# Kernel tuning notes

Hardware: AMD Instinct MI355X
Metric: run time of the kernel (lower is better)

## Reference

```python
import jax, jax.numpy as jnp
import numpy as np
import math

EPS = 1e-7
K_NEIGHBORS = 32  # matches init kwarg k

def _project(x, c):
    norm = jnp.linalg.norm(x, axis=-1, keepdims=True).clip(EPS)
    sqrt_c = jnp.sqrt(c).clip(EPS)
    max_norm = (1.0 - EPS) / sqrt_c
    return x * jnp.minimum(max_norm / norm, 1.0)

def _mobius_add(x, y, c):
    x2 = jnp.sum(x * x, axis=-1, keepdims=True)
    y2 = jnp.sum(y * y, axis=-1, keepdims=True)
    xy = jnp.sum(x * y, axis=-1, keepdims=True)
    num = (1 + 2 * c * xy + c * y2) * x + (1 - c * x2) * y
    den = 1 + 2 * c * xy + c * c * x2 * y2
    return _project(num / den.clip(EPS), c)

def _dist(x, y, c):
    sqrt_c = jnp.sqrt(c).clip(EPS)
    diff = _mobius_add(x, -y, c)
    dn = jnp.linalg.norm(diff, axis=-1)
    arg = jnp.minimum(sqrt_c * dn.clip(EPS, 1 - EPS), 1.0 - EPS)
    return 2.0 * jnp.arctanh(arg) / sqrt_c

def _logmap0(y, c):
    sqrt_c = jnp.sqrt(c).clip(EPS)
    yn = jnp.linalg.norm(y, axis=-1, keepdims=True)
    is_zero = yn < EPS
    syn = yn.clip(EPS)
    arg = jnp.minimum(sqrt_c * syn, 1.0 - EPS)
    mag = jnp.arctanh(arg) / sqrt_c
    return jnp.where(is_zero, jnp.zeros_like(y), mag * y / syn)

def _layernorm(x, g, b):
    m = x.mean(-1, keepdims=True)
    v = x.var(-1, keepdims=True)
    return (x - m) / jnp.sqrt(v + 1e-6) * g + b

def setup_inputs() -> dict:
    key = jax.random.key(0)
    B, N, D, P, H = 2, 2048, 512, 3, 8
    ks = jax.random.split(key, 16)
    s = 0.02
    d = {}
    d['x'] = jax.random.normal(ks[0], (B, N, D), dtype=jnp.float32)
    d['positions'] = jax.random.normal(ks[1], (B, N, P), dtype=jnp.float32) * 0.1
    d['c'] = jnp.float32(1.0)
    d['Wq'] = jax.random.normal(ks[2], (D, D), jnp.float32) * s; d['bq'] = jnp.zeros((D,), jnp.float32)
    d['Wk'] = jax.random.normal(ks[3], (D, D), jnp.float32) * s; d['bk'] = jnp.zeros((D,), jnp.float32)
    d['Wv'] = jax.random.normal(ks[4], (D, D), jnp.float32) * s; d['bv'] = jnp.zeros((D,), jnp.float32)
    d['Wg'] = jax.random.normal(ks[5], (P, D), jnp.float32) * s; d['bg'] = jnp.zeros((D,), jnp.float32)
    d['Wo'] = jax.random.normal(ks[6], (D, D), jnp.float32) * s; d['bo'] = jnp.zeros((D,), jnp.float32)
    d['Wf1'] = jax.random.normal(ks[7], (D, 4 * D), jnp.float32) * s; d['bf1'] = jnp.zeros((4 * D,), jnp.float32)
    d['Wf2'] = jax.random.normal(ks[8], (4 * D, D), jnp.float32) * s; d['bf2'] = jnp.zeros((D,), jnp.float32)
    d['g1'] = jnp.ones((D,), jnp.float32); d['b1'] = jnp.zeros((D,), jnp.float32)
    d['g2'] = jnp.ones((D,), jnp.float32); d['b2'] = jnp.zeros((D,), jnp.float32)
    d['ascale'] = jnp.ones((H,), jnp.float32)
    d['fscale'] = jnp.ones((H,), jnp.float32)
    return d

def reference(x, positions, c, Wq, bq, Wk, bk, Wv, bv, Wg, bg, Wo, bo, Wf1, bf1, Wf2, bf2, g1, b1, g2, b2, ascale, fscale):
    B, N, D = x.shape
    H = ascale.shape[0]
    hd = D // H
    K = K_NEIGHBORS

    xn = _layernorm(x, g1, b1)
    q = (xn @ Wq + bq).reshape(B, N, H, hd)
    k = (xn @ Wk + bk).reshape(B, N, H, hd)
    v = (xn @ Wv + bv).reshape(B, N, H, hd)

    # full pairwise hyperbolic distance matrix [B, N, N]
    dmat = _dist(positions[:, :, None, :], positions[:, None, :, :], c)
    idx = jax.lax.top_k(-dmat, K)[1]  # [B, N, K]

    bidx = jnp.arange(B)[:, None, None]
    key_pos = positions[bidx, idx]                 # [B, N, K, P]
    qpos = positions[:, :, None, :]                # [B, N, 1, P]
    geo = _logmap0(_mobius_add(-qpos, key_pos, c), c)
    geo_v = (geo @ Wg + bg).reshape(B, N, K, H, hd)

    kg = k[bidx, idx]                              # [B, N, K, H, hd]
    vg = v[bidx, idx]

    align = jnp.einsum('bnhd,bnkhd->bhnk', q, geo_v)
    feat = jnp.einsum('bnhd,bnkhd->bhnk', q, kg) / math.sqrt(hd)
    scores = fscale[None, :, None, None] * feat + ascale[None, :, None, None] * align
    w = jax.nn.softmax(scores.astype(jnp.float32), axis=-1)
    attn = jnp.einsum('bhnk,bnkhd->bnhd', w, vg).reshape(B, N, D)

    x1 = x + attn @ Wo + bo
    h = _layernorm(x1, g2, b2)
    x2 = x1 + jax.nn.gelu(h @ Wf1 + bf1) @ Wf2 + bf2
    return x2
```

## Files before the change

### kernel.cpp

```cpp
#include <hip/hip_runtime.h>
#include <math.h>

#define EPSF 1e-7f

constexpr int Bb = 2, Nn = 2048, Dd = 512, Hh = 8, HD = 64, KK = 32;
constexpr int ROWS = Bb * Nn;

typedef __attribute__((ext_vector_type(8))) short bf16x8;
typedef __attribute__((ext_vector_type(4))) float f32x4;
typedef __attribute__((ext_vector_type(8))) unsigned short u16x8;
typedef unsigned long long u64;

__device__ inline unsigned short f2bf(float f) {
    union { float f; unsigned int u; } v; v.f = f;
    unsigned int u = v.u;
    unsigned int r = (u + 0x7fffu + ((u >> 16) & 1u)) >> 16;
    return (unsigned short)r;
}

__device__ inline float bf2f(short s) {
    union { unsigned int u; float f; } x;
    x.u = ((unsigned int)(unsigned short)s) << 16;
    return x.f;
}

__device__ inline float gelu_tanh(float v) {
    float u = v + 0.044715f * v * v * v;
    return 0.5f * v * (1.f + tanhf(0.79788456080286535588f * u));
}

__device__ __forceinline__ void tcvt(float (*tile)[65], const float* __restrict__ in,
                                     unsigned short* __restrict__ out,
                                     int K, int N, int bx, int by) {
    int k0 = by * 64, n0 = bx * 64;
    int t = threadIdx.x;
    int lr = t >> 6, lc = t & 63;
#pragma unroll 4
    for (int p = 0; p < 16; ++p) {
        int r = p * 4 + lr;
        tile[r][lc] = in[(size_t)(k0 + r) * N + n0 + lc];
    }
    __syncthreads();
#pragma unroll 4
    for (int p = 0; p < 16; ++p) {
        int n = p * 4 + lr;
        out[(size_t)(n0 + n) * K + k0 + lc] = f2bf(tile[lc][n]);
    }
}

__device__ __forceinline__ void ln_row(const float* __restrict__ x,
                                       const float* __restrict__ g,
                                       const float* __restrict__ b,
                                       unsigned short* __restrict__ out,
                                       int row, int lane) {
    const float* xr = x + (size_t)row * Dd;
    float4 v0 = *(const float4*)(xr + lane * 8);
    float4 v1 = *(const float4*)(xr + lane * 8 + 4);
    float s = v0.x + v0.y + v0.z + v0.w + v1.x + v1.y + v1.z + v1.w;
    float s2 = v0.x * v0.x + v0.y * v0.y + v0.z * v0.z + v0.w * v0.w +
               v1.x * v1.x + v1.y * v1.y + v1.z * v1.z + v1.w * v1.w;
    for (int o = 32; o; o >>= 1) { s += __shfl_xor(s, o); s2 += __shfl_xor(s2, o); }
    float mean = s * (1.f / Dd);
    float var = s2 * (1.f / Dd) - mean * mean;
    float rstd = rsqrtf(var + 1e-6f);
    float4 g0 = *(const float4*)(g + lane * 8);
    float4 g1v = *(const float4*)(g + lane * 8 + 4);
    float4 b0 = *(const float4*)(b + lane * 8);
    float4 b1v = *(const float4*)(b + lane * 8 + 4);
    u16x8 o;
    o[0] = f2bf((v0.x - mean) * rstd * g0.x + b0.x);
    o[1] = f2bf((v0.y - mean) * rstd * g0.y + b0.y);
    o[2] = f2bf((v0.z - mean) * rstd * g0.z + b0.z);
    o[3] = f2bf((v0.w - mean) * rstd * g0.w + b0.w);
    o[4] = f2bf((v1.x - mean) * rstd * g1v.x + b1v.x);
    o[5] = f2bf((v1.y - mean) * rstd * g1v.y + b1v.y);
    o[6] = f2bf((v1.z - mean) * rstd * g1v.z + b1v.z);
    o[7] = f2bf((v1.w - mean) * rstd * g1v.w + b1v.w);
    *(u16x8*)(out + (size_t)row * Dd + lane * 8) = o;
}

__global__ __launch_bounds__(256) void ln_kernel(const float* __restrict__ x,
                                                 const float* __restrict__ g,
                                                 const float* __restrict__ b,
                                                 unsigned short* __restrict__ out) {
    ln_row(x, g, b, out, blockIdx.x * 4 + (threadIdx.x >> 6), threadIdx.x & 63);
}

__global__ __launch_bounds__(256) void prep_kernel(
    const float* __restrict__ Wq, const float* __restrict__ Wk,
    const float* __restrict__ Wv, const float* __restrict__ Wo,
    const float* __restrict__ Wf1, const float* __restrict__ Wf2,
    const float* __restrict__ bq, const float* __restrict__ bk, const float* __restrict__ bv,
    const float* __restrict__ x, const float* __restrict__ g1, const float* __restrict__ b1,
    unsigned short* __restrict__ wqkv_t, unsigned short* __restrict__ wo_t,
    unsigned short* __restrict__ wf1_t, unsigned short* __restrict__ wf2_t,
    float* __restrict__ bqkv, unsigned short* __restrict__ xn) {
    __shared__ float tile[64][65];
    int bid = blockIdx.x;
    if (bid < 256) {
        int z = bid >> 6, r = bid & 63;
        const float* in = (z == 0) ? Wq : (z == 1) ? Wk : (z == 2) ? Wv : Wo;
        unsigned short* out = (z == 0) ? wqkv_t : (z == 1) ? wqkv_t + 262144
                            : (z == 2) ? wqkv_t + 524288 : wo_t;
        tcvt(tile, in, out, 512, 512, r & 7, r >> 3);
    } else if (bid < 512) {
        int r = bid - 256;
        tcvt(tile, Wf1, wf1_t, 512, 2048, r & 31, r >> 5);
    } else if (bid < 768) {
        int r = bid - 512;
        tcvt(tile, Wf2, wf2_t, 2048, 512, r & 7, r >> 3);
    } else if (bid < 774) {
        int t = (bid - 768) * 256 + threadIdx.x;
        if (t < 512) bqkv[t] = bq[t];
        else if (t < 1024) bqkv[t] = bk[t - 512];
        else if (t < 1536) bqkv[t] = bv[t - 1024];
    } else {
        ln_row(x, g1, b1, xn, (bid - 774) * 4 + (threadIdx.x >> 6), threadIdx.x & 63);
    }
}

template <int EPI, int OBF16>
__global__ __launch_bounds__(256) void gemm64(const unsigned short* __restrict__ A,
                                              const unsigned short* __restrict__ Bt,
                                              const float* __restrict__ bias,
                                              const float* __restrict__ resid,
                                              void* __restrict__ C,
                                              int N, int K, int gridX) {
    __shared__ short As[2 * 64 * 64];
    __shared__ short Bs[2 * 64 * 64];
    int nwg = gridDim.x;
    int cpx = nwg >> 3;
    int wgid = blockIdx.x;
    int nid = (wgid & 7) * cpx + (wgid >> 3);
    int bx = nid % gridX, by = nid / gridX;
    int bm = by * 64, bn = bx * 64;
    int tid = threadIdx.x;
    int wave = tid >> 6, lane = tid & 63;
    int wr = wave >> 1, wc = wave & 1;
    f32x4 acc[2][2] = {};

    int srow = wave * 8 + (lane >> 3);
    int scol = ((lane & 7) ^ (lane >> 3)) * 8;
    const unsigned short* gA0 = A + (size_t)(bm + srow) * K + scol;
    const unsigned short* gA1 = A + (size_t)(bm + srow + 32) * K + scol;
    const unsigned short* gB0 = Bt + (size_t)(bn + srow) * K + scol;
    const unsigned short* gB1 = Bt + (size_t)(bn + srow + 32) * K + scol;

#define STAGE(buf, kof)                                                                                 \
    do {                                                                                                \
        __builtin_amdgcn_global_load_lds((const __attribute__((address_space(1))) void*)(gA0 + (kof)), \
            (__attribute__((address_space(3))) void*)(As + (buf) * 4096 + wave * 512), 16, 0, 0);       \
        __builtin_amdgcn_global_load_lds((const __attribute__((address_space(1))) void*)(gA1 + (kof)), \
            (__attribute__((address_space(3))) void*)(As + (buf) * 4096 + 2048 + wave * 512), 16, 0, 0);\
        __builtin_amdgcn_global_load_lds((const __attribute__((address_space(1))) void*)(gB0 + (kof)), \
            (__attribute__((address_space(3))) void*)(Bs + (buf) * 4096 + wave * 512), 16, 0, 0);       \
        __builtin_amdgcn_global_load_lds((const __attribute__((address_space(1))) void*)(gB1 + (kof)), \
            (__attribute__((address_space(3))) void*)(Bs + (buf) * 4096 + 2048 + wave * 512), 16, 0, 0);\
    } while (0)

    int nt = K >> 6;
    int cur = 0;
    STAGE(0, 0);
    __syncthreads();
    for (int t = 0; t < nt; ++t) {
        if (t + 1 < nt) STAGE(cur ^ 1, (t + 1) * 64);
        const short* as = As + cur * 4096;
        const short* bs = Bs + cur * 4096;
#pragma unroll
        for (int kk = 0; kk < 64; kk += 32) {
            int kx = (kk + (lane >> 4) * 8) ^ ((lane & 7) << 3);
            bf16x8 a0 = *(const bf16x8*)(as + (wr * 32 + (lane & 15)) * 64 + kx);
            bf16x8 a1 = *(const bf16x8*)(as + (wr * 32 + 16 + (lane & 15)) * 64 + kx);
            bf16x8 b0 = *(const bf16x8*)(bs + (wc * 32 + (lane & 15)) * 64 + kx);
            bf16x8 b1 = *(const bf16x8*)(bs + (wc * 32 + 16 + (lane & 15)) * 64 + kx);
            acc[0][0] = __builtin_amdgcn_mfma_f32_16x16x32_bf16(a0, b0, acc[0][0], 0, 0, 0);
            acc[0][1] = __builtin_amdgcn_mfma_f32_16x16x32_bf16(a0, b1, acc[0][1], 0, 0, 0);
            acc[1][0] = __builtin_amdgcn_mfma_f32_16x16x32_bf16(a1, b0, acc[1][0], 0, 0, 0);
            acc[1][1] = __builtin_amdgcn_mfma_f32_16x16x32_bf16(a1, b1, acc[1][1], 0, 0, 0);
        }
        __syncthreads();
        cur ^= 1;
    }
#undef STAGE

    int cbase = bn + wc * 32 + (lane & 15);
    int rbase = bm + wr * 32 + (lane >> 4) * 4;
    float bias_v[2] = {bias[cbase], bias[cbase + 16]};
#pragma unroll
    for (int mi = 0; mi < 2; ++mi) {
#pragma unroll
        for (int r = 0; r < 4; ++r) {
            int row = rbase + mi * 16 + r;
#pragma unroll
            for (int ni = 0; ni < 2; ++ni) {
                int col = cbase + ni * 16;
                float v = acc[mi][ni][r] + bias_v[ni];
                if (EPI == 1) v += resid[(size_t)row * N + col];
                if (EPI == 2) v = gelu_tanh(v);
                if (OBF16) ((unsigned short*)C)[(size_t)row * N + col] = f2bf(v);
                else ((float*)C)[(size_t)row * N + col] = v;
            }
        }
    }
}

template <int CTRL>
__device__ inline float dpp_f(float v) {
    int i = __float_as_int(v);
    i = __builtin_amdgcn_update_dpp(i, i, CTRL, 0xF, 0xF, false);
    return __int_as_float(i);
}
template <int CTRL>
__device__ inline unsigned dpp_u(unsigned v) {
    return (unsigned)__builtin_amdgcn_update_dpp((int)v, (int)v, CTRL, 0xF, 0xF, false);
}

__device__ inline float wave_min_f32(float v) {
    v = fminf(v, dpp_f<0xB1>(v));
    v = fminf(v, dpp_f<0x4E>(v));
    v = fminf(v, dpp_f<0x141>(v));
    v = fminf(v, dpp_f<0x140>(v));
    v = fminf(v, __shfl_xor(v, 16));
    v = fminf(v, __shfl_xor(v, 32));
    return v;
}
__device__ inline unsigned wave_min_u32(unsigned v) {
    unsigned o;
    o = dpp_u<0xB1>(v);  v = o < v ? o : v;
    o = dpp_u<0x4E>(v);  v = o < v ? o : v;
    o = dpp_u<0x141>(v); v = o < v ? o : v;
    o = dpp_u<0x140>(v); v = o < v ? o : v;
    o = __shfl_xor(v, 16); v = o < v ? o : v;
    o = __shfl_xor(v, 32); v = o < v ? o : v;
    return v;
}

__global__ __launch_bounds__(256, 4) void topk_kernel(const float* __restrict__ pos,
                                                      const float* __restrict__ cp,
                                                      int* __restrict__ idx_out) {
    __shared__ float s_px[Nn], s_py[Nn], s_pz[Nn], s_u[Nn];
    __shared__ int s_out[4][KK];
    int b = blockIdx.x >> 9;
    int q0 = (blockIdx.x & 511) * 4;
    int t = threadIdx.x;
    float c = *cp;
    const float* pb = pos + (size_t)b * Nn * 3;
    for (int j = t; j < Nn; j += 256) {
        float px = pb[j * 3 + 0], py = pb[j * 3 + 1], pz = pb[j * 3 + 2];
        s_px[j] = px; s_py[j] = py; s_pz[j] = pz;
        s_u[j] = c * (px * px + py * py + pz * pz);
    }
    __syncthreads();
    int wave = t >> 6, lane = t & 63;
    int n = q0 + wave;
    float qx = s_px[n], qy = s_py[n], qz = s_pz[n];
    float cx2 = s_u[n];
    float x2 = cx2 / c;
    float B = 1.f - cx2;
    float rc = 1.f / c;
    float B2rc = B * B * rc;
    float m2c = -2.f * c;
    float m2B = -2.f * B;
    float key[32];
#pragma unroll
    for (int i = 0; i < 32; ++i) {
        int j = i * 64 + lane;
        float dot = qx * s_px[j] + qy * s_py[j] + qz * s_pz[j];
        float su = s_u[j];
        float r = fmaf(m2c, dot, 1.f);
        float A = r + su;
        float den = fmaf(cx2, su, r);
        float p1 = x2 * A;
        float q1 = A * dot;
        float t1 = fmaf(m2B, q1, B2rc * su);
        float num2 = fmaf(p1, A, t1);
        float rd = __builtin_amdgcn_rcpf(den);
        key[i] = fmaf(num2, rd * rd, 1.0f);
    }
    const u64 MAXK = ~0ull;
    u64 B0 = MAXK, B1 = MAXK, B2 = MAXK, B3 = MAXK;
#pragma unroll
    for (int i = 0; i < 32; ++i) {
        u64 k = ((u64)__float_as_uint(key[i]) << 32) | (unsigned int)(i * 64 + lane);
        if (k < B3) {
            B3 = k;
            if (B3 < B2) { u64 tmp = B2; B2 = B3; B3 = tmp; }
            if (B2 < B1) { u64 tmp = B1; B1 = B2; B2 = tmp; }
            if (B1 < B0) { u64 tmp = B0; B0 = B1; B1 = tmp; }
        }
    }
    int bcount = 4, consumed = 0;
    u64 last = 0;
    for (int s2 = 0; s2 < KK; ++s2) {
        bool need = (bcount == 0) && (consumed < 32);
        if (__any(need)) {
            if (need) {
                B0 = MAXK; B1 = MAXK; B2 = MAXK; B3 = MAXK;
#pragma unroll
                for (int i = 0; i < 32; ++i) {
                    u64 k = ((u64)__float_as_uint(key[i]) << 32) | (unsigned int)(i * 64 + lane);
                    if (k > last && k < B3) {
                        B3 = k;
                        if (B3 < B2) { u64 tmp = B2; B2 = B3; B3 = tmp; }
                        if (B2 < B1) { u64 tmp = B1; B1 = B2; B2 = tmp; }
                        if (B1 < B0) { u64 tmp = B0; B0 = B1; B1 = tmp; }
                    }
                }
                int rem = 32 - consumed;
                bcount = rem < 4 ? rem : 4;
            }
        }
        u64 offer = (bcount > 0) ? B0 : MAXK;
        float okey = __uint_as_float((unsigned)(offer >> 32));
        unsigned oidx = (unsigned)offer;
        float m = wave_min_f32(okey);
        u64 mask = __ballot(okey == m);
        unsigned gidx;
        if (__popcll(mask) == 1) {
            gidx = (unsigned)__shfl((int)oidx, __ffsll(mask) - 1);
        } else {
            unsigned cand = ((mask >> lane) & 1ull) ? oidx : 0xFFFFFFFFu;
            gidx = wave_min_u32(cand);
        }
        if (lane == 0) s_out[wave][s2] = (int)gidx;
        if (okey == m && oidx == gidx) {
            B0 = B1; B1 = B2; B2 = B3; B3 = MAXK;
            --bcount; ++consumed;
            last = ((u64)__float_as_uint(m) << 32) | gidx;
        }
    }
    if (lane < KK) idx_out[(size_t)(b * Nn + n) * KK + lane] = s_out[wave][lane];
}

__global__ __launch_bounds__(256) void attn_kernel(const unsigned short* __restrict__ qkv,
                                                   const int* __restrict__ idx,
                                                   const float* __restrict__ pos,
                                                   const float* __restrict__ Wg,
                                                   const float* __restrict__ bg,
                                                   const float* __restrict__ ascale,
                                                   const float* __restrict__ fscale,
                                                   const float* __restrict__ cp,
                                                   unsigned short* __restrict__ out) {
    constexpr int QS = 1536;
    int bid = blockIdx.x;
    int xcd = bid & 7, slot = bid >> 3;
    int b = xcd >> 2;
    int n = (xcd & 3) * 512 + slot;
    int bn = b * Nn + n;
    int t = threadIdx.x;
    int wave = t >> 6, lane = t & 63;
    __shared__ float s_q[Dd];
    __shared__ float s_geo[KK][3];
    __shared__ int s_idx[KK];
    __shared__ float s_qg[Hh][3];
    __shared__ float s_qb[Hh];
    __shared__ float s_dot[KK][9];
    __shared__ float s_w[Hh][KK];
    __shared__ float s_part[4][Dd];
    float c = *cp;
    if (t >= 64 && t < 96) s_idx[t - 64] = idx[(size_t)bn * KK + (t - 64)];
    if (t < 64) {
        bf16x8 q8 = *(const bf16x8*)(qkv + (size_t)bn * QS + t * 8);
#pragma unroll
        for (int j = 0; j < 8; ++j) s_q[t * 8 + j] = bf2f(q8[j]);
    }
    __syncthreads();
    if (t < KK) {
        const float* qp = pos + (size_t)bn * 3;
        const float* kp = pos + (size_t)(b * Nn + s_idx[t]) * 3;
        float xx = -qp[0], xyc = -qp[1], xz = -qp[2];
        float yx = kp[0], yy = kp[1], yz = kp[2];
        float x2 = xx * xx + xyc * xyc + xz * xz;
        float y2 = yx * yx + yy * yy + yz * yz;
        float xy = xx * yx + xyc * yy + xz * yz;
        float Av = 1.f + 2.f * c * xy + c * y2;
        float Bv = 1.f - c * x2;
        float den = fmaxf(1.f + 2.f * c * xy + c * c * x2 * y2, EPSF);
        float mx = (Av * xx + Bv * yx) / den;
        float my = (Av * xyc + Bv * yy) / den;
        float mz = (Av * xz + Bv * yz) / den;
        float rn = fmaxf(sqrtf(mx * mx + my * my + mz * mz), EPSF);
        float sqrt_c = fmaxf(sqrtf(c), EPSF);
        float max_norm = (1.f - EPSF) / sqrt_c;
        float scpr = fminf(max_norm / rn, 1.f);
        mx *= scpr; my *= scpr; mz *= scpr;
        float yn = sqrtf(mx * mx + my * my + mz * mz);
        if (yn < EPSF) {
            s_geo[t][0] = 0.f; s_geo[t][1] = 0.f; s_geo[t][2] = 0.f;
        } else {
            float syn = fmaxf(yn, EPSF);
            float arg = fminf(sqrt_c * syn, 1.f - EPSF);
            float mag = atanhf(arg) / sqrt_c;
            float f = mag / syn;
            s_geo[t][0] = mx * f; s_geo[t][1] = my * f; s_geo[t][2] = mz * f;
        }
    } else if (t >= 64 && t < 88) {
        int h = (t - 64) / 3, p = (t - 64) % 3;
        float acc = 0.f;
        for (int d2 = 0; d2 < HD; ++d2) acc += s_q[h * HD + d2] * Wg[p * Dd + h * HD + d2];
        s_qg[h][p] = acc;
    } else if (t >= 96 && t < 104) {
        int h = t - 96;
        float acc = 0.f;
        for (int d2 = 0; d2 < HD; ++d2) acc += s_q[h * HD + d2] * bg[h * HD + d2];
        s_qb[h] = acc;
    }
    bf16x8 v8r[8];
    {
#pragma unroll
        for (int r = 0; r < 8; ++r) {
            int kk = wave * 8 + r;
            int nk = s_idx[kk];
            bf16x8 k8 = *(const bf16x8*)(qkv + (size_t)(b * Nn + nk) * QS + 512 + lane * 8);
            float p = 0.f;
#pragma unroll
            for (int j = 0; j < 8; ++j) p = fmaf(bf2f(k8[j]), s_q[lane * 8 + j], p);
            p += __shfl_xor(p, 1);
            p += __shfl_xor(p, 2);
            p += __shfl_xor(p, 4);
            if ((lane & 7) == 0) s_dot[kk][lane >> 3] = p;
        }
#pragma unroll
        for (int r = 0; r < 8; ++r) {
            int nk = s_idx[wave * 8 + r];
            v8r[r] = *(const bf16x8*)(qkv + (size_t)(b * Nn + nk) * QS + 1024 + lane * 8);
        }
    }
    __syncthreads();
    {
        int h = t >> 5, kk = t & 31;
        float align = s_geo[kk][0] * s_qg[h][0] + s_geo[kk][1] * s_qg[h][1] +
                      s_geo[kk][2] * s_qg[h][2] + s_qb[h];
        float scv = fscale[h] * s_dot[kk][h] * 0.125f + ascale[h] * align;
        float m = scv;
        for (int o = 16; o; o >>= 1) m = fmaxf(m, __shfl_xor(m, o));
        float e = expf(scv - m);
        float ss = e;
        for (int o = 16; o; o >>= 1) ss += __shfl_xor(ss, o);
        s_w[h][kk] = e / ss;
    }
    __syncthreads();
    {
        float acc[8] = {0.f, 0.f, 0.f, 0.f, 0.f, 0.f, 0.f, 0.f};
        int h = lane >> 3;
#pragma unroll
        for (int r = 0; r < 8; ++r) {
            float wgt = s_w[h][wave * 8 + r];
#pragma unroll
            for (int j = 0; j < 8; ++j) acc[j] = fmaf(bf2f(v8r[r][j]), wgt, acc[j]);
        }
#pragma unroll
        for (int j = 0; j < 8; ++j) s_part[wave][lane * 8 + j] = acc[j];
    }
    __syncthreads();
    for (int d = t; d < Dd; d += 256) {
        float s = s_part[0][d] + s_part[1][d] + s_part[2][d] + s_part[3][d];
        out[(size_t)bn * Dd + d] = f2bf(s);
    }
}

extern "C" void kernel_launch(void* const* d_in, const int* in_sizes, int n_in,
                              void* d_out, int out_size, void* d_ws, size_t ws_size,
                              hipStream_t stream) {
    const float* x   = (const float*)d_in[0];
    const float* pos = (const float*)d_in[1];
    const float* cp  = (const float*)d_in[2];
    const float* Wq  = (const float*)d_in[3];
    const float* bq  = (const float*)d_in[4];
    const float* Wk  = (const float*)d_in[5];
    const float* bk  = (const float*)d_in[6];
    const float* Wv  = (const float*)d_in[7];
    const float* bv  = (const float*)d_in[8];
    const float* Wg  = (const float*)d_in[9];
    const float* bg  = (const float*)d_in[10];
    const float* Wo  = (const float*)d_in[11];
    const float* bo  = (const float*)d_in[12];
    const float* Wf1 = (const float*)d_in[13];
    const float* bf1 = (const float*)d_in[14];
    const float* Wf2 = (const float*)d_in[15];
    const float* bf2 = (const float*)d_in[16];
    const float* g1  = (const float*)d_in[17];
    const float* b1  = (const float*)d_in[18];
    const float* g2  = (const float*)d_in[19];
    const float* b2  = (const float*)d_in[20];
    const float* asc = (const float*)d_in[21];
    const float* fsc = (const float*)d_in[22];
    float* out = (float*)d_out;
    char* ws = (char*)d_ws;

    unsigned short* qkv_bf  = (unsigned short*)(ws + 0);
    unsigned short* t_bf    = (unsigned short*)(ws + 0);
    unsigned short* xn_bf   = (unsigned short*)(ws + 25165824);
    float*          x1      = (float*)(ws + 29360128);
    unsigned short* attn_bf = (unsigned short*)(ws + 37748736);
    unsigned short* wqkv_t  = (unsigned short*)(ws + 41943040);
    unsigned short* wo_t    = (unsigned short*)(ws + 43515904);
    unsigned short* wf1_t   = (unsigned short*)(ws + 44040192);
    unsigned short* wf2_t   = (unsigned short*)(ws + 46137344);
    int*            idx     = (int*)(ws + 48234496);
    float*          bqkv    = (float*)(ws + 48758784);

    prep_kernel<<<1798, 256, 0, stream>>>(Wq, Wk, Wv, Wo, Wf1, Wf2, bq, bk, bv,
                                          x, g1, b1, wqkv_t, wo_t, wf1_t, wf2_t, bqkv, xn_bf);
    topk_kernel<<<ROWS / 4, 256, 0, stream>>>(pos, cp, idx);
    gemm64<0, 1><<<1536, 256, 0, stream>>>(xn_bf, wqkv_t, bqkv, nullptr, qkv_bf, 1536, 512, 24);
    attn_kernel<<<ROWS, 256, 0, stream>>>(qkv_bf, idx, pos, Wg, bg, asc, fsc, cp, attn_bf);
    gemm64<1, 0><<<512, 256, 0, stream>>>(attn_bf, wo_t, bo, x, x1, 512, 512, 8);
    ln_kernel<<<ROWS / 4, 256, 0, stream>>>(x1, g2, b2, xn_bf);
    gemm64<2, 1><<<2048, 256, 0, stream>>>(xn_bf, wf1_t, bf1, nullptr, t_bf, 2048, 512, 32);
    gemm64<1, 0><<<512, 256, 0, stream>>>(t_bf, wf2_t, bf2, x1, out, 512, 2048, 8);
}
```

Baseline: 138.9 us.

## Fuse top-k into prep kernel and use 128x64 tiles for wide GEMMs

Merges the neighbor top-k selection into the weight-prep/layernorm launch as extra blocks, removing one kernel launch and letting the two independent stages run side by side. Adds a 128x64 GEMM tile variant, used for the QKV and FFN-up projections, so each A/B tile loaded into LDS feeds more MFMAs. The fused kernel now reserves about 33KB of shared memory for every block and sets a min-4-blocks launch bound, which may limit occupancy for the prep blocks. The larger tile halves the grid size and raises register pressure.

```diff
diff --git a/kernel.cpp b/kernel.cpp
--- a/kernel.cpp
+++ b/kernel.cpp
@@ -86,7 +86,138 @@
     ln_row(x, g, b, out, blockIdx.x * 4 + (threadIdx.x >> 6), threadIdx.x & 63);
 }
 
-__global__ __launch_bounds__(256) void prep_kernel(
+template <int CTRL>
+__device__ inline float dpp_f(float v) {
+    int i = __float_as_int(v);
+    i = __builtin_amdgcn_update_dpp(i, i, CTRL, 0xF, 0xF, false);
+    return __int_as_float(i);
+}
+template <int CTRL>
+__device__ inline unsigned dpp_u(unsigned v) {
+    return (unsigned)__builtin_amdgcn_update_dpp((int)v, (int)v, CTRL, 0xF, 0xF, false);
+}
+
+__device__ inline float wave_min_f32(float v) {
+    v = fminf(v, dpp_f<0xB1>(v));
+    v = fminf(v, dpp_f<0x4E>(v));
+    v = fminf(v, dpp_f<0x141>(v));
+    v = fminf(v, dpp_f<0x140>(v));
+    v = fminf(v, __shfl_xor(v, 16));
+    v = fminf(v, __shfl_xor(v, 32));
+    return v;
+}
+__device__ inline unsigned wave_min_u32(unsigned v) {
+    unsigned o;
+    o = dpp_u<0xB1>(v);  v = o < v ? o : v;
+    o = dpp_u<0x4E>(v);  v = o < v ? o : v;
+    o = dpp_u<0x141>(v); v = o < v ? o : v;
+    o = dpp_u<0x140>(v); v = o < v ? o : v;
+    o = __shfl_xor(v, 16); v = o < v ? o : v;
+    o = __shfl_xor(v, 32); v = o < v ? o : v;
+    return v;
+}
+
+__device__ __forceinline__ void topk_body(char* smem, const float* __restrict__ pos,
+                                          const float* __restrict__ cp,
+                                          int* __restrict__ idx_out, int bid) {
+    float* s_px = (float*)smem;
+    float* s_py = s_px + Nn;
+    float* s_pz = s_py + Nn;
+    float* s_u  = s_pz + Nn;
+    int* s_out  = (int*)(s_u + Nn);
+    int b = bid >> 9;
+    int q0 = (bid & 511) * 4;
+    int t = threadIdx.x;
+    float c = *cp;
+    const float* pb = pos + (size_t)b * Nn * 3;
+    for (int j = t; j < Nn; j += 256) {
+        float px = pb[j * 3 + 0], py = pb[j * 3 + 1], pz = pb[j * 3 + 2];
+        s_px[j] = px; s_py[j] = py; s_pz[j] = pz;
+        s_u[j] = c * (px * px + py * py + pz * pz);
+    }
+    __syncthreads();
+    int wave = t >> 6, lane = t & 63;
+    int n = q0 + wave;
+    float qx = s_px[n], qy = s_py[n], qz = s_pz[n];
+    float cx2 = s_u[n];
+    float x2 = cx2 / c;
+    float B = 1.f - cx2;
+    float rc = 1.f / c;
+    float B2rc = B * B * rc;
+    float m2c = -2.f * c;
+    float m2B = -2.f * B;
+    float key[32];
+#pragma unroll
+    for (int i = 0; i < 32; ++i) {
+        int j = i * 64 + lane;
+        float dot = qx * s_px[j] + qy * s_py[j] + qz * s_pz[j];
+        float su = s_u[j];
+        float r = fmaf(m2c, dot, 1.f);
+        float A = r + su;
+        float den = fmaf(cx2, su, r);
+        float p1 = x2 * A;
+        float q1 = A * dot;
+        float t1 = fmaf(m2B, q1, B2rc * su);
+        float num2 = fmaf(p1, A, t1);
+        float rd = __builtin_amdgcn_rcpf(den);
+        key[i] = fmaf(num2, rd * rd, 1.0f);
+    }
+    const u64 MAXK = ~0ull;
+    u64 B0 = MAXK, B1 = MAXK, B2 = MAXK, B3 = MAXK;
+#pragma unroll
+    for (int i = 0; i < 32; ++i) {
+        u64 k = ((u64)__float_as_uint(key[i]) << 32) | (unsigned int)(i * 64 + lane);
+        if (k < B3) {
+            B3 = k;
+            if (B3 < B2) { u64 tmp = B2; B2 = B3; B3 = tmp; }
+            if (B2 < B1) { u64 tmp = B1; B1 = B2; B2 = tmp; }
+            if (B1 < B0) { u64 tmp = B0; B0 = B1; B1 = tmp; }
+        }
+    }
+    int bcount = 4, consumed = 0;
+    u64 last = 0;
+    for (int s2 = 0; s2 < KK; ++s2) {
+        bool need = (bcount == 0) && (consumed < 32);
+        if (__any(need)) {
+            if (need) {
+                B0 = MAXK; B1 = MAXK; B2 = MAXK; B3 = MAXK;
+#pragma unroll
+                for (int i = 0; i < 32; ++i) {
+                    u64 k = ((u64)__float_as_uint(key[i]) << 32) | (unsigned int)(i * 64 + lane);
+                    if (k > last && k < B3) {
+                        B3 = k;
+                        if (B3 < B2) { u64 tmp = B2; B2 = B3; B3 = tmp; }
+                        if (B2 < B1) { u64 tmp = B1; B1 = B2; B2 = tmp; }
+                        if (B1 < B0) { u64 tmp = B0; B0 = B1; B1 = tmp; }
+                    }
+                }
+                int rem = 32 - consumed;
+                bcount = rem < 4 ? rem : 4;
+            }
+        }
+        u64 offer = (bcount > 0) ? B0 : MAXK;
+        float okey = __uint_as_float((unsigned)(offer >> 32));
+        unsigned oidx = (unsigned)offer;
+        float m = wave_min_f32(okey);
+        u64 mask = __ballot(okey == m);
+        unsigned gidx;
+        if (__popcll(mask) == 1) {
+            gidx = (unsigned)__shfl((int)oidx, __ffsll(mask) - 1);
+        } else {
+            unsigned cand = ((mask >> lane) & 1ull) ? oidx : 0xFFFFFFFFu;
+            gidx = wave_min_u32(cand);
+        }
+        if (lane == 0) s_out[wave * KK + s2] = (int)gidx;
+        if (okey == m && oidx == gidx) {
+            B0 = B1; B1 = B2; B2 = B3; B3 = MAXK;
+            --bcount; ++consumed;
+            last = ((u64)__float_as_uint(m) << 32) | gidx;
+        }
+    }
+    if (lane < KK) idx_out[(size_t)(b * Nn + n) * KK + lane] = s_out[wave * KK + lane];
+}
+
+__global__ __launch_bounds__(256, 4) void prep_topk_kernel(
     const float* __restrict__ Wq, const float* __restrict__ Wk,
     const float* __restrict__ Wv, const float* __restrict__ Wo,
     const float* __restrict__ Wf1, const float* __restrict__ Wf2,
@@ -94,9 +225,15 @@
     const float* __restrict__ x, const float* __restrict__ g1, const float* __restrict__ b1,
     unsigned short* __restrict__ wqkv_t, unsigned short* __restrict__ wo_t,
     unsigned short* __restrict__ wf1_t, unsigned short* __restrict__ wf2_t,
-    float* __restrict__ bqkv, unsigned short* __restrict__ xn) {
-    __shared__ float tile[64][65];
+    float* __restrict__ bqkv, unsigned short* __restrict__ xn,
+    const float* __restrict__ pos, const float* __restrict__ cp, int* __restrict__ idx_out) {
+    __shared__ __align__(16) char smem[33280];
     int bid = blockIdx.x;
+    if (bid >= 1798) {
+        topk_body(smem, pos, cp, idx_out, bid - 1798);
+        return;
+    }
+    float (*tile)[65] = (float (*)[65])smem;
     if (bid < 256) {
         int z = bid >> 6, r = bid & 63;
         const float* in = (z == 0) ? Wq : (z == 1) ? Wk : (z == 2) ? Wv : Wo;
@@ -120,6 +257,97 @@
 }
 
 template <int EPI, int OBF16>
+__global__ __launch_bounds__(256) void gemm128x64(const unsigned short* __restrict__ A,
+                                                  const unsigned short* __restrict__ Bt,
+                                                  const float* __restrict__ bias,
+                                                  const float* __restrict__ resid,
+                                                  void* __restrict__ C,
+                                                  int N, int K, int gridX) {
+    __shared__ short As[2 * 128 * 64];
+    __shared__ short Bs[2 * 64 * 64];
+    int nwg = gridDim.x;
+    int cpx = nwg >> 3;
+    int wgid = blockIdx.x;
+    int nid = (wgid & 7) * cpx + (wgid >> 3);
+    int bx = nid % gridX, by = nid / gridX;
+    int bm = by * 128, bn = bx * 64;
+    int tid = threadIdx.x;
+    int wave = tid >> 6, lane = tid & 63;
+    int wr = wave >> 1, wc = wave & 1;
+    f32x4 acc[4][2] = {};
+
+    int srow = wave * 8 + (lane >> 3);
+    int scol = ((lane & 7) ^ (lane >> 3)) * 8;
+
+#define STAGE(buf, kof)                                                                                   \
+    do {                                                                                                  \
+        _Pragma("unroll")                                                                                 \
+        for (int cc = 0; cc < 4; ++cc) {                                                                  \
+            const unsigned short* ga = A + (size_t)(bm + cc * 32 + srow) * K + (kof) + scol;              \
+            __builtin_amdgcn_global_load_lds((const __attribute__((address_space(1))) void*)ga,          \
+                (__attribute__((address_space(3))) void*)(As + (buf) * 8192 + cc * 2048 + wave * 512),    \
+                16, 0, 0);                                                                                \
+        }                                                                                                 \
+        _Pragma("unroll")                                                                                 \
+        for (int cc = 0; cc < 2; ++cc) {                                                                  \
+            const unsigned short* gb = Bt + (size_t)(bn + cc * 32 + srow) * K + (kof) + scol;             \
+            __builtin_amdgcn_global_load_lds((const __attribute__((address_space(1))) void*)gb,          \
+                (__attribute__((address_space(3))) void*)(Bs + (buf) * 4096 + cc * 2048 + wave * 512),    \
+                16, 0, 0);                                                                                \
+        }                                                                                                 \
+    } while (0)
+
+    int nt = K >> 6;
+    int cur = 0;
+    STAGE(0, 0);
+    __syncthreads();
+    for (int t = 0; t < nt; ++t) {
+        if (t + 1 < nt) STAGE(cur ^ 1, (t + 1) * 64);
+        const short* as = As + cur * 8192;
+        const short* bs = Bs + cur * 4096;
+#pragma unroll
+        for (int kk = 0; kk < 64; kk += 32) {
+            int kx = (kk + (lane >> 4) * 8) ^ ((lane & 7) << 3);
+            bf16x8 af[4], bfr[2];
+#pragma unroll
+            for (int mi = 0; mi < 4; ++mi)
+                af[mi] = *(const bf16x8*)(as + (wr * 64 + mi * 16 + (lane & 15)) * 64 + kx);
+#pragma unroll
+            for (int ni = 0; ni < 2; ++ni)
+                bfr[ni] = *(const bf16x8*)(bs + (wc * 32 + ni * 16 + (lane & 15)) * 64 + kx);
+#pragma unroll
+            for (int mi = 0; mi < 4; ++mi)
+#pragma unroll
+                for (int ni = 0; ni < 2; ++ni)
+                    acc[mi][ni] = __builtin_amdgcn_mfma_f32_16x16x32_bf16(af[mi], bfr[ni], acc[mi][ni], 0, 0, 0);
+        }
+        __syncthreads();
+        cur ^= 1;
+    }
+#undef STAGE
+
+    int cbase = bn + wc * 32 + (lane & 15);
+    int rbase = bm + wr * 64 + (lane >> 4) * 4;
+    float bias_v[2] = {bias[cbase], bias[cbase + 16]};
+#pragma unroll
+    for (int mi = 0; mi < 4; ++mi) {
+#pragma unroll
+        for (int r = 0; r < 4; ++r) {
+            int row = rbase + mi * 16 + r;
+#pragma unroll
+            for (int ni = 0; ni < 2; ++ni) {
+                int col = cbase + ni * 16;
+                float v = acc[mi][ni][r] + bias_v[ni];
+                if (EPI == 1) v += resid[(size_t)row * N + col];
+                if (EPI == 2) v = gelu_tanh(v);
+                if (OBF16) ((unsigned short*)C)[(size_t)row * N + col] = f2bf(v);
+                else ((float*)C)[(size_t)row * N + col] = v;
+            }
+        }
+    }
+}
+
+template <int EPI, int OBF16>
 __global__ __launch_bounds__(256) void gemm64(const unsigned short* __restrict__ A,
                                               const unsigned short* __restrict__ Bt,
                                               const float* __restrict__ bias,
@@ -202,134 +430,6 @@
             }
         }
     }
-}
-
-template <int CTRL>
-__device__ inline float dpp_f(float v) {
-    int i = __float_as_int(v);
-    i = __builtin_amdgcn_update_dpp(i, i, CTRL, 0xF, 0xF, false);
-    return __int_as_float(i);
-}
-template <int CTRL>
-__device__ inline unsigned dpp_u(unsigned v) {
-    return (unsigned)__builtin_amdgcn_update_dpp((int)v, (int)v, CTRL, 0xF, 0xF, false);
-}
-
-__device__ inline float wave_min_f32(float v) {
-    v = fminf(v, dpp_f<0xB1>(v));
-    v = fminf(v, dpp_f<0x4E>(v));
-    v = fminf(v, dpp_f<0x141>(v));
-    v = fminf(v, dpp_f<0x140>(v));
-    v = fminf(v, __shfl_xor(v, 16));
-    v = fminf(v, __shfl_xor(v, 32));
-    return v;
-}
-__device__ inline unsigned wave_min_u32(unsigned v) {
-    unsigned o;
-    o = dpp_u<0xB1>(v);  v = o < v ? o : v;
-    o = dpp_u<0x4E>(v);  v = o < v ? o : v;
-    o = dpp_u<0x141>(v); v = o < v ? o : v;
-    o = dpp_u<0x140>(v); v = o < v ? o : v;
-    o = __shfl_xor(v, 16); v = o < v ? o : v;
-    o = __shfl_xor(v, 32); v = o < v ? o : v;
-    return v;
-}
-
-__global__ __launch_bounds__(256, 4) void topk_kernel(const float* __restrict__ pos,
-                                                      const float* __restrict__ cp,
-                                                      int* __restrict__ idx_out) {
-    __shared__ float s_px[Nn], s_py[Nn], s_pz[Nn], s_u[Nn];
-    __shared__ int s_out[4][KK];
-    int b = blockIdx.x >> 9;
-    int q0 = (blockIdx.x & 511) * 4;
-    int t = threadIdx.x;
-    float c = *cp;
-    const float* pb = pos + (size_t)b * Nn * 3;
-    for (int j = t; j < Nn; j += 256) {
-        float px = pb[j * 3 + 0], py = pb[j * 3 + 1], pz = pb[j * 3 + 2];
-        s_px[j] = px; s_py[j] = py; s_pz[j] = pz;
-        s_u[j] = c * (px * px + py * py + pz * pz);
-    }
-    __syncthreads();
-    int wave = t >> 6, lane = t & 63;
-    int n = q0 + wave;
-    float qx = s_px[n], qy = s_py[n], qz = s_pz[n];
-    float cx2 = s_u[n];
-    float x2 = cx2 / c;
-    float B = 1.f - cx2;
-    float rc = 1.f / c;
-    float B2rc = B * B * rc;
-    float m2c = -2.f * c;
-    float m2B = -2.f * B;
-    float key[32];
-#pragma unroll
-    for (int i = 0; i < 32; ++i) {
-        int j = i * 64 + lane;
-        float dot = qx * s_px[j] + qy * s_py[j] + qz * s_pz[j];
-        float su = s_u[j];
-        float r = fmaf(m2c, dot, 1.f);
-        float A = r + su;
-        float den = fmaf(cx2, su, r);
-        float p1 = x2 * A;
-        float q1 = A * dot;
-        float t1 = fmaf(m2B, q1, B2rc * su);
-        float num2 = fmaf(p1, A, t1);
-        float rd = __builtin_amdgcn_rcpf(den);
-        key[i] = fmaf(num2, rd * rd, 1.0f);
-    }
-    const u64 MAXK = ~0ull;
-    u64 B0 = MAXK, B1 = MAXK, B2 = MAXK, B3 = MAXK;
-#pragma unroll
-    for (int i = 0; i < 32; ++i) {
-        u64 k = ((u64)__float_as_uint(key[i]) << 32) | (unsigned int)(i * 64 + lane);
-        if (k < B3) {
-            B3 = k;
-            if (B3 < B2) { u64 tmp = B2; B2 = B3; B3 = tmp; }
-            if (B2 < B1) { u64 tmp = B1; B1 = B2; B2 = tmp; }
-            if (B1 < B0) { u64 tmp = B0; B0 = B1; B1 = tmp; }
-        }
-    }
-    int bcount = 4, consumed = 0;
-    u64 last = 0;
-    for (int s2 = 0; s2 < KK; ++s2) {
-        bool need = (bcount == 0) && (consumed < 32);
-        if (__any(need)) {
-            if (need) {
-                B0 = MAXK; B1 = MAXK; B2 = MAXK; B3 = MAXK;
-#pragma unroll
-                for (int i = 0; i < 32; ++i) {
-                    u64 k = ((u64)__float_as_uint(key[i]) << 32) | (unsigned int)(i * 64 + lane);
-                    if (k > last && k < B3) {
-                        B3 = k;
-                        if (B3 < B2) { u64 tmp = B2; B2 = B3; B3 = tmp; }
-                        if (B2 < B1) { u64 tmp = B1; B1 = B2; B2 = tmp; }
-                        if (B1 < B0) { u64 tmp = B0; B0 = B1; B1 = tmp; }
-                    }
-                }
-                int rem = 32 - consumed;
-                bcount = rem < 4 ? rem : 4;
-            }
-        }
-        u64 offer = (bcount > 0) ? B0 : MAXK;
-        float okey = __uint_as_float((unsigned)(offer >> 32));
-        unsigned oidx = (unsigned)offer;
-        float m = wave_min_f32(okey);
-        u64 mask = __ballot(okey == m);
-        unsigned gidx;
-        if (__popcll(mask) == 1) {
-            gidx = (unsigned)__shfl((int)oidx, __ffsll(mask) - 1);
-        } else {
-            unsigned cand = ((mask >> lane) & 1ull) ? oidx : 0xFFFFFFFFu;
-            gidx = wave_min_u32(cand);
-        }
-        if (lane == 0) s_out[wave][s2] = (int)gidx;
-        if (okey == m && oidx == gidx) {
-            B0 = B1; B1 = B2; B2 = B3; B3 = MAXK;
-            --bcount; ++consumed;
-            last = ((u64)__float_as_uint(m) << 32) | gidx;
-        }
-    }
-    if (lane < KK) idx_out[(size_t)(b * Nn + n) * KK + lane] = s_out[wave][lane];
 }
 
 __global__ __launch_bounds__(256) void attn_kernel(const unsigned short* __restrict__ qkv,
@@ -500,13 +600,13 @@
     int*            idx     = (int*)(ws + 48234496);
     float*          bqkv    = (float*)(ws + 48758784);
 
-    prep_kernel<<<1798, 256, 0, stream>>>(Wq, Wk, Wv, Wo, Wf1, Wf2, bq, bk, bv,
-                                          x, g1, b1, wqkv_t, wo_t, wf1_t, wf2_t, bqkv, xn_bf);
-    topk_kernel<<<ROWS / 4, 256, 0, stream>>>(pos, cp, idx);
-    gemm64<0, 1><<<1536, 256, 0, stream>>>(xn_bf, wqkv_t, bqkv, nullptr, qkv_bf, 1536, 512, 24);
+    prep_topk_kernel<<<1798 + 1024, 256, 0, stream>>>(
+        Wq, Wk, Wv, Wo, Wf1, Wf2, bq, bk, bv, x, g1, b1,
+        wqkv_t, wo_t, wf1_t, wf2_t, bqkv, xn_bf, pos, cp, idx);
+    gemm128x64<0, 1><<<768, 256, 0, stream>>>(xn_bf, wqkv_t, bqkv, nullptr, qkv_bf, 1536, 512, 24);
     attn_kernel<<<ROWS, 256, 0, stream>>>(qkv_bf, idx, pos, Wg, bg, asc, fsc, cp, attn_bf);
     gemm64<1, 0><<<512, 256, 0, stream>>>(attn_bf, wo_t, bo, x, x1, 512, 512, 8);
     ln_kernel<<<ROWS / 4, 256, 0, stream>>>(x1, g2, b2, xn_bf);
-    gemm64<2, 1><<<2048, 256, 0, stream>>>(xn_bf, wf1_t, bf1, nullptr, t_bf, 2048, 512, 32);
+    gemm128x64<2, 1><<<1024, 256, 0, stream>>>(xn_bf, wf1_t, bf1, nullptr, t_bf, 2048, 512, 32);
     gemm64<1, 0><<<512, 256, 0, stream>>>(t_bf, wf2_t, bf2, x1, out, 512, 2048, 8);
 }
```

Measured after the change: 134.3 us. -3.4%, faster.
